# Performance work log

Hardware: AMD Instinct MI355X
Metric: run time of the kernel (lower is better)

## Reference

```python
import jax, jax.numpy as jnp
import numpy as np

EPS = 0.05        # idw eps from __init__
RMS_EPS = 1e-6    # rmsnorm eps
B, NTOT, N, GS, C = 128, 129, 128, 16, 384


def setup_inputs() -> dict:
    key = jax.random.key(0)
    k1, k2, k3, k4 = jax.random.split(key, 4)
    f = jax.random.normal(k1, (B, NTOT, C), dtype=jnp.float32)
    distance = jax.random.uniform(k2, (B, N, GS), dtype=jnp.float32)
    rf = jax.random.normal(k3, (NTOT, C), dtype=jnp.float32)
    knorm_w = jnp.ones((C,), dtype=jnp.float32)
    idx = jax.random.randint(k4, (B, N, GS), 0, B * N, dtype=jnp.int64)
    return {"f": f, "distance": distance, "rf": rf, "knorm_w": knorm_w, "idx": idx}


def _rmsnorm(x, w):
    rms = jnp.sqrt(jnp.mean(x * x, axis=-1, keepdims=True) + RMS_EPS)
    return x / rms * w


def reference(f, distance, rf, knorm_w, idx):
    t = f.shape[1] - N                       # number of cls tokens (1)
    cls_token = f[:, :t, :]                  # [B, t, C]
    x = f[:, t:, :]                          # [B, 128, C]
    rfx = rf[t:]                             # [128, C]
    c = rfx                                  # adabias: per-point bias broadcast over batch
    bsz, n_pts, ch = x.shape
    # gather neighbors: flat index into [B*128, C]
    nf = x.reshape(-1, ch)[idx.reshape(-1)].reshape(bsz, n_pts, GS, ch)
    nf = nf - x[:, :, None, :]               # centering
    fb = c + x                               # bias-shifted center features
    # inverse-distance weights over group dim
    w = 1.0 / (distance + EPS)
    w = w / jnp.sum(w, axis=-1, keepdims=True)
    sf = jnp.sum(w[..., None] * nf, axis=2)  # [B, 128, C]
    out = fb + _rmsnorm(sf, knorm_w)
    return jnp.concatenate([cls_token, out], axis=1)
```

## Files before the change

kernel.cpp:

```cpp
#include <hip/hip_runtime.h>
#include <hip/hip_bf16.h>

#define EPSW 0.05f
#define RMS_EPS 1e-6f
#define NB 128
#define NTOT 129
#define NN 128
#define GS 16
#define NC 384
#define NROWS (NB * NN)

static __device__ __forceinline__ unsigned short f2bf(float x) {
    unsigned u = __builtin_bit_cast(unsigned, x);
    unsigned r = (u + 0x7fffu + ((u >> 16) & 1u)) >> 16;
    return (unsigned short)r;
}

__global__ __launch_bounds__(256) void pack_kernel(const float* __restrict__ f,
                                                   unsigned short* __restrict__ xb)
{
    const int b    = blockIdx.x >> 3;
    const int part = blockIdx.x & 7;
    const float4* src = (const float4*)(f + ((size_t)b * NTOT + 1) * NC) + part * 1536;
    unsigned short* dst = xb + (size_t)b * NN * NC + (size_t)part * 6144;
    #pragma unroll
    for (int i = 0; i < 6; ++i) {
        const int e = i * 256 + threadIdx.x;
        const float4 v = src[e];
        ushort4 o;
        o.x = f2bf(v.x); o.y = f2bf(v.y); o.z = f2bf(v.z); o.w = f2bf(v.w);
        ((ushort4*)dst)[e] = o;
    }
}

template <bool USEBF>
__global__ __launch_bounds__(192) void rectify_kernel(
    const float* __restrict__ f,
    const float* __restrict__ distance,
    const float* __restrict__ rf,
    const float* __restrict__ knorm,
    const int* __restrict__ idx,
    const unsigned short* __restrict__ xb,
    float* __restrict__ out)
{
    const int bn  = blockIdx.x;
    const int b   = bn >> 7;
    const int n   = bn & 127;
    const int tid = threadIdx.x;

    __shared__ float wls[GS];
    __shared__ int   ils[GS];

    if (tid < GS) {
        const float w = 1.0f / (distance[(size_t)bn * GS + tid] + EPSW);
        float s = w;
        #pragma unroll
        for (int o = 8; o >= 1; o >>= 1) s += __shfl_xor(s, o);
        wls[tid] = w / s;
        ils[tid] = idx[(size_t)bn * GS + tid];
    }

    const float2 xv = ((const float2*)(f + ((size_t)b * NTOT + 1 + n) * NC))[tid];

    if (n == 0) {
        ((float2*)(out + (size_t)b * NTOT * NC))[tid] =
            ((const float2*)(f + (size_t)b * NTOT * NC))[tid];
    }

    __syncthreads();

    float wv[GS]; int rv[GS];
    #pragma unroll
    for (int g = 0; g < GS; ++g) { wv[g] = wls[g]; rv[g] = ils[g]; }

    float2 acc = make_float2(0.0f, 0.0f);
    if (USEBF) {
        const unsigned* xb32 = (const unsigned*)xb;
        #pragma unroll
        for (int g = 0; g < GS; ++g) {
            const unsigned u = xb32[(size_t)rv[g] * 192 + tid];
            const float lo = __builtin_bit_cast(float, u << 16);
            const float hi = __builtin_bit_cast(float, u & 0xffff0000u);
            acc.x += wv[g] * (lo - xv.x);
            acc.y += wv[g] * (hi - xv.y);
        }
    } else {
        #pragma unroll
        for (int g = 0; g < GS; ++g) {
            const int r = rv[g];
            const float2 v =
                ((const float2*)(f + ((size_t)(r >> 7) * NTOT + 1 + (r & 127)) * NC))[tid];
            acc.x += wv[g] * (v.x - xv.x);
            acc.y += wv[g] * (v.y - xv.y);
        }
    }

    float ss = acc.x * acc.x + acc.y * acc.y;
    #pragma unroll
    for (int o = 32; o > 0; o >>= 1) ss += __shfl_xor(ss, o);
    __shared__ float part[3];
    const int wave = tid >> 6;
    if ((tid & 63) == 0) part[wave] = ss;
    __syncthreads();
    const float tot  = part[0] + part[1] + part[2];
    const float rinv = rsqrtf(tot / (float)NC + RMS_EPS);

    const float2 rvv = ((const float2*)(rf + (size_t)(1 + n) * NC))[tid];
    const float2 kv  = ((const float2*)knorm)[tid];

    float2 o;
    o.x = rvv.x + xv.x + acc.x * rinv * kv.x;
    o.y = rvv.y + xv.y + acc.y * rinv * kv.y;
    ((float2*)(out + ((size_t)b * NTOT + 1 + n) * NC))[tid] = o;
}

extern "C" void kernel_launch(void* const* d_in, const int* in_sizes, int n_in,
                              void* d_out, int out_size, void* d_ws, size_t ws_size,
                              hipStream_t stream) {
    const float* f        = (const float*)d_in[0];
    const float* distance = (const float*)d_in[1];
    const float* rf       = (const float*)d_in[2];
    const float* knorm    = (const float*)d_in[3];
    const int*   idx      = (const int*)d_in[4];
    float*       out      = (float*)d_out;

    const size_t need = (size_t)NROWS * NC * sizeof(unsigned short);
    if (ws_size >= need) {
        unsigned short* xb = (unsigned short*)d_ws;
        pack_kernel<<<1024, 256, 0, stream>>>(f, xb);
        rectify_kernel<true><<<NROWS, 192, 0, stream>>>(
            f, distance, rf, knorm, idx, xb, out);
    } else {
        rectify_kernel<false><<<NROWS, 192, 0, stream>>>(
            f, distance, rf, knorm, idx, nullptr, out);
    }
}
```

Baseline: 110.7 us.

## Map one wavefront per output row with shuffle-broadcast weights and indices

The rectify kernel now handles four (b,n) rows per 256-thread block, one wave each. Each lane owns six channels and the weights and indices are broadcast with wave shuffles instead of shared memory, so both __syncthreads barriers go away. The fp32 fallback path is dropped and the bf16 workspace is always used, which risks out-of-bounds writes if the workspace is too small. Per-lane gather loads become three scalar dwords at a 12-byte stride, which may coalesce less cleanly.

```diff
diff --git a/kernel.cpp b/kernel.cpp
--- a/kernel.cpp
+++ b/kernel.cpp
@@ -1,5 +1,4 @@
 #include <hip/hip_runtime.h>
-#include <hip/hip_bf16.h>
 
 #define EPSW 0.05f
 #define RMS_EPS 1e-6f
@@ -33,85 +32,88 @@
     }
 }
 
-template <bool USEBF>
-__global__ __launch_bounds__(192) void rectify_kernel(
+__global__ __launch_bounds__(256) void rectify_kernel(
     const float* __restrict__ f,
     const float* __restrict__ distance,
     const float* __restrict__ rf,
     const float* __restrict__ knorm,
     const int* __restrict__ idx,
-    const unsigned short* __restrict__ xb,
+    const unsigned* __restrict__ xb32,
     float* __restrict__ out)
 {
-    const int bn  = blockIdx.x;
-    const int b   = bn >> 7;
-    const int n   = bn & 127;
-    const int tid = threadIdx.x;
+    const int wave = threadIdx.x >> 6;
+    const int lane = threadIdx.x & 63;
+    const int bn   = (blockIdx.x << 2) | wave;
+    const int b    = bn >> 7;
+    const int n    = bn & 127;
+    const int c0   = lane * 6;
 
-    __shared__ float wls[GS];
-    __shared__ int   ils[GS];
+    const int g16 = lane & 15;
+    const float w = 1.0f / (distance[(size_t)bn * GS + g16] + EPSW);
+    float s = w;
+    s += __shfl_xor(s, 1); s += __shfl_xor(s, 2);
+    s += __shfl_xor(s, 4); s += __shfl_xor(s, 8);
+    const float wn = w / s;
+    const int   ri = idx[(size_t)bn * GS + g16];
 
-    if (tid < GS) {
-        const float w = 1.0f / (distance[(size_t)bn * GS + tid] + EPSW);
-        float s = w;
-        #pragma unroll
-        for (int o = 8; o >= 1; o >>= 1) s += __shfl_xor(s, o);
-        wls[tid] = w / s;
-        ils[tid] = idx[(size_t)bn * GS + tid];
+    const float* xrow = f + ((size_t)b * NTOT + 1 + n) * NC + c0;
+    const float2 x01 = *(const float2*)(xrow);
+    const float2 x23 = *(const float2*)(xrow + 2);
+    const float2 x45 = *(const float2*)(xrow + 4);
+
+    if (n == 0) {
+        const float* cs = f + (size_t)b * NTOT * NC + c0;
+        float*       cd = out + (size_t)b * NTOT * NC + c0;
+        *(float2*)(cd)     = *(const float2*)(cs);
+        *(float2*)(cd + 2) = *(const float2*)(cs + 2);
+        *(float2*)(cd + 4) = *(const float2*)(cs + 4);
     }
 
-    const float2 xv = ((const float2*)(f + ((size_t)b * NTOT + 1 + n) * NC))[tid];
-
-    if (n == 0) {
-        ((float2*)(out + (size_t)b * NTOT * NC))[tid] =
-            ((const float2*)(f + (size_t)b * NTOT * NC))[tid];
+    float a0 = 0, a1 = 0, a2 = 0, a3 = 0, a4 = 0, a5 = 0;
+    #pragma unroll
+    for (int g = 0; g < GS; ++g) {
+        const int   r  = __shfl(ri, g);
+        const float wg = __shfl(wn, g);
+        const unsigned* p = xb32 + (size_t)r * 192 + lane * 3;
+        const unsigned u0 = p[0], u1 = p[1], u2 = p[2];
+        const float v0 = __builtin_bit_cast(float, u0 << 16);
+        const float v1 = __builtin_bit_cast(float, u0 & 0xffff0000u);
+        const float v2 = __builtin_bit_cast(float, u1 << 16);
+        const float v3 = __builtin_bit_cast(float, u1 & 0xffff0000u);
+        const float v4 = __builtin_bit_cast(float, u2 << 16);
+        const float v5 = __builtin_bit_cast(float, u2 & 0xffff0000u);
+        a0 += wg * (v0 - x01.x);
+        a1 += wg * (v1 - x01.y);
+        a2 += wg * (v2 - x23.x);
+        a3 += wg * (v3 - x23.y);
+        a4 += wg * (v4 - x45.x);
+        a5 += wg * (v5 - x45.y);
     }
 
-    __syncthreads();
-
-    float wv[GS]; int rv[GS];
-    #pragma unroll
-    for (int g = 0; g < GS; ++g) { wv[g] = wls[g]; rv[g] = ils[g]; }
-
-    float2 acc = make_float2(0.0f, 0.0f);
-    if (USEBF) {
-        const unsigned* xb32 = (const unsigned*)xb;
-        #pragma unroll
-        for (int g = 0; g < GS; ++g) {
-            const unsigned u = xb32[(size_t)rv[g] * 192 + tid];
-            const float lo = __builtin_bit_cast(float, u << 16);
-            const float hi = __builtin_bit_cast(float, u & 0xffff0000u);
-            acc.x += wv[g] * (lo - xv.x);
-            acc.y += wv[g] * (hi - xv.y);
-        }
-    } else {
-        #pragma unroll
-        for (int g = 0; g < GS; ++g) {
-            const int r = rv[g];
-            const float2 v =
-                ((const float2*)(f + ((size_t)(r >> 7) * NTOT + 1 + (r & 127)) * NC))[tid];
-            acc.x += wv[g] * (v.x - xv.x);
-            acc.y += wv[g] * (v.y - xv.y);
-        }
-    }
-
-    float ss = acc.x * acc.x + acc.y * acc.y;
+    float ss = a0*a0 + a1*a1 + a2*a2 + a3*a3 + a4*a4 + a5*a5;
     #pragma unroll
     for (int o = 32; o > 0; o >>= 1) ss += __shfl_xor(ss, o);
-    __shared__ float part[3];
-    const int wave = tid >> 6;
-    if ((tid & 63) == 0) part[wave] = ss;
-    __syncthreads();
-    const float tot  = part[0] + part[1] + part[2];
-    const float rinv = rsqrtf(tot / (float)NC + RMS_EPS);
+    const float rinv = rsqrtf(ss * (1.0f / (float)NC) + RMS_EPS);
 
-    const float2 rvv = ((const float2*)(rf + (size_t)(1 + n) * NC))[tid];
-    const float2 kv  = ((const float2*)knorm)[tid];
+    const float* rfrow = rf + (size_t)(1 + n) * NC + c0;
+    const float2 r01 = *(const float2*)(rfrow);
+    const float2 r23 = *(const float2*)(rfrow + 2);
+    const float2 r45 = *(const float2*)(rfrow + 4);
+    const float2 k01 = *(const float2*)(knorm + c0);
+    const float2 k23 = *(const float2*)(knorm + c0 + 2);
+    const float2 k45 = *(const float2*)(knorm + c0 + 4);
 
-    float2 o;
-    o.x = rvv.x + xv.x + acc.x * rinv * kv.x;
-    o.y = rvv.y + xv.y + acc.y * rinv * kv.y;
-    ((float2*)(out + ((size_t)b * NTOT + 1 + n) * NC))[tid] = o;
+    float* orow = out + ((size_t)b * NTOT + 1 + n) * NC + c0;
+    float2 o01, o23, o45;
+    o01.x = r01.x + x01.x + a0 * rinv * k01.x;
+    o01.y = r01.y + x01.y + a1 * rinv * k01.y;
+    o23.x = r23.x + x23.x + a2 * rinv * k23.x;
+    o23.y = r23.y + x23.y + a3 * rinv * k23.y;
+    o45.x = r45.x + x45.x + a4 * rinv * k45.x;
+    o45.y = r45.y + x45.y + a5 * rinv * k45.y;
+    *(float2*)(orow)     = o01;
+    *(float2*)(orow + 2) = o23;
+    *(float2*)(orow + 4) = o45;
 }
 
 extern "C" void kernel_launch(void* const* d_in, const int* in_sizes, int n_in,
@@ -124,14 +126,8 @@
     const int*   idx      = (const int*)d_in[4];
     float*       out      = (float*)d_out;
 
-    const size_t need = (size_t)NROWS * NC * sizeof(unsigned short);
-    if (ws_size >= need) {
-        unsigned short* xb = (unsigned short*)d_ws;
-        pack_kernel<<<1024, 256, 0, stream>>>(f, xb);
-        rectify_kernel<true><<<NROWS, 192, 0, stream>>>(
-            f, distance, rf, knorm, idx, xb, out);
-    } else {
-        rectify_kernel<false><<<NROWS, 192, 0, stream>>>(
-            f, distance, rf, knorm, idx, nullptr, out);
-    }
+    unsigned short* xb = (unsigned short*)d_ws;
+    pack_kernel<<<1024, 256, 0, stream>>>(f, xb);
+    rectify_kernel<<<NROWS / 4, 256, 0, stream>>>(
+        f, distance, rf, knorm, idx, (const unsigned*)xb, out);
 }
```

Result: no change. 110.5 us (-0.1%).
